# Performance work log

Measured on AMD Instinct MI355X. Metric: run time of the kernel, lower is better.

## Reference

```python
import jax, jax.numpy as jnp
import numpy as np

N = 100000      # nodes
E = 3200000     # edges
G = 128         # graphs in batch
D_IN = 128
D_H = 256
D_OUT = 64
BN_EPS = 1e-3


def setup_inputs() -> dict:
    key = jax.random.key(0)
    ks = jax.random.split(key, 12)
    h = jax.random.normal(ks[0], (N, D_IN), jnp.float32)
    src = jax.random.randint(ks[1], (E,), 0, N, jnp.int32)
    dst = jax.random.randint(ks[2], (E,), 0, N, jnp.int32)
    graph_ids = jnp.sort(jax.random.randint(ks[3], (N,), 0, G, jnp.int32))
    # GraphConv weights (DGL default: weight + bias)
    W0 = jax.random.normal(ks[4], (D_IN, D_H), jnp.float32) * 0.05
    b0 = jnp.zeros((D_H,), jnp.float32)
    W = jax.random.normal(ks[5], (2, D_H, D_H), jnp.float32) * 0.05  # layers 1,2
    b = jnp.zeros((2, D_H), jnp.float32)
    # BatchNorm1d params (eval mode: running stats), 3 norm layers
    bn_gamma = jnp.ones((3, D_H), jnp.float32)
    bn_beta = jnp.zeros((3, D_H), jnp.float32)
    bn_mean = jax.random.normal(ks[6], (3, D_H), jnp.float32) * 0.1
    bn_var = jax.random.uniform(ks[7], (3, D_H), jnp.float32, 0.5, 1.5)
    # prediction head
    Wp = jax.random.normal(ks[8], (D_H, D_OUT), jnp.float32) * 0.05
    bp = jnp.zeros((D_OUT,), jnp.float32)
    return {"h": h, "W0": W0, "b0": b0, "W": W, "b": b,
            "bn_gamma": bn_gamma, "bn_beta": bn_beta, "bn_mean": bn_mean,
            "bn_var": bn_var, "Wp": Wp, "bp": bp,
            "src": src, "dst": dst, "graph_ids": graph_ids}


def reference(h, W0, b0, W, b, bn_gamma, bn_beta, bn_mean, bn_var, Wp, bp,
              src, dst, graph_ids):
    n = h.shape[0]
    ones_e = jnp.ones(src.shape, h.dtype)
    # symmetric normalization (DGL GraphConv norm='both'), degrees clamped to 1
    out_deg = jax.ops.segment_sum(ones_e, src, num_segments=n)
    in_deg = jax.ops.segment_sum(ones_e, dst, num_segments=n)
    norm_src = jax.lax.rsqrt(jnp.clip(out_deg, 1.0))  # [N]
    norm_dst = jax.lax.rsqrt(jnp.clip(in_deg, 1.0))   # [N]

    def graph_conv(x, Wl, bl):
        x = (x * norm_src[:, None]) @ Wl              # transform first (mult W then aggregate)
        agg = jax.ops.segment_sum(x[src], dst, num_segments=n)  # SpMM: gather+scatter-add
        return agg * norm_dst[:, None] + bl

    Ws = [W0, W[0], W[1]]
    bs = [b0, b[0], b[1]]
    for i in range(3):
        x = h
        h = graph_conv(h, Ws[i], bs[i])
        # BatchNorm1d in eval mode (running stats), eps=1e-3
        h = (h - bn_mean[i]) * jax.lax.rsqrt(bn_var[i] + BN_EPS) * bn_gamma[i] + bn_beta[i]
        h = jax.nn.relu(h) + (x if i != 0 else 0.0)   # residual skipped on first layer

    # mean pooling per graph
    counts = jax.ops.segment_sum(jnp.ones((n,), h.dtype), graph_ids, num_segments=G)
    pooled = jax.ops.segment_sum(h, graph_ids, num_segments=G) / jnp.clip(counts, 1.0)[:, None]
    return pooled @ Wp + bp
```

## Files before the change

### kernel.cpp

```cpp
#include <hip/hip_runtime.h>
#include <hip/hip_bf16.h>

#define NN 100000
#define EE 3200000
#define GG 128
#define D_IN 128
#define D_H 256
#define D_OUT 64
#define BN_EPS 1e-3f
#define PAD 96
#define LDSTRIDE 40
#define X8SCALE 16.0f
#define X8INV   0.0625f

#define NBUCK 782
#define BUCKET_CAP 5120
#define EPT 8

#define GEMM_NWG 1564

typedef __hip_bfloat16 bf16;
typedef __attribute__((ext_vector_type(8))) short short8;
typedef __attribute__((ext_vector_type(4))) float float4v;
typedef __attribute__((ext_vector_type(2))) float float2v;
typedef __attribute__((ext_vector_type(4))) int intv4;
typedef __attribute__((ext_vector_type(4))) unsigned short usv4;

#if __has_builtin(__builtin_amdgcn_cvt_pk_f32_fp8) && __has_builtin(__builtin_amdgcn_cvt_pk_fp8_f32)
#define HAVE_FP8_CVT 1
#endif

__device__ inline float h2f(unsigned short s) {
    _Float16 h; __builtin_memcpy(&h, &s, 2); return (float)h;
}
__device__ inline unsigned short f2h(float f) {
    _Float16 h = (_Float16)f; unsigned short s; __builtin_memcpy(&s, &h, 2); return s;
}
__device__ inline float4 load4h(const unsigned short* p) {
    ushort4 u = *(const ushort4*)p;
    return make_float4(h2f(u.x), h2f(u.y), h2f(u.z), h2f(u.w));
}
__device__ inline void store4h(unsigned short* p, float4 v) {
    ushort4 u;
    u.x = f2h(v.x); u.y = f2h(v.y); u.z = f2h(v.z); u.w = f2h(v.w);
    *(ushort4*)p = u;
}
__device__ inline float4 load4h_nt(const unsigned short* p) {
    usv4 u = __builtin_nontemporal_load((const usv4*)p);
    return make_float4(h2f(u.x), h2f(u.y), h2f(u.z), h2f(u.w));
}

__device__ inline unsigned char enc_fp8(float f) {
#ifdef HAVE_FP8_CVT
    int r = __builtin_amdgcn_cvt_pk_fp8_f32(f, f, 0, false);
    return (unsigned char)(r & 0xFF);
#else
    union { float f; unsigned u; } c; c.f = f;
    unsigned s = (c.u >> 31) << 7;
    float a = fabsf(f);
    if (!(a >= 0.015625f)) {
        int q = (int)rintf(a * 512.0f);
        return (unsigned char)(s | (unsigned)q);
    }
    if (a >= 464.0f) return (unsigned char)(s | 0x7E);
    int e = (int)((c.u >> 23) & 0xFF) - 127;
    int q = (int)rintf(ldexpf(a, 3 - e));
    if (q == 16) { q = 8; e += 1; }
    return (unsigned char)(s | ((unsigned)(e + 7) << 3) | (unsigned)(q - 8));
#endif
}
__device__ inline unsigned int enc4_fp8(float4 v) {
#ifdef HAVE_FP8_CVT
    int r = __builtin_amdgcn_cvt_pk_fp8_f32(v.x, v.y, 0, false);
    r = __builtin_amdgcn_cvt_pk_fp8_f32(v.z, v.w, r, true);
    return (unsigned int)r;
#else
    return (unsigned int)enc_fp8(v.x) | ((unsigned int)enc_fp8(v.y) << 8)
         | ((unsigned int)enc_fp8(v.z) << 16) | ((unsigned int)enc_fp8(v.w) << 24);
#endif
}
__device__ inline float4 dec4_fp8(unsigned int w) {
#ifdef HAVE_FP8_CVT
    float2v lo = __builtin_amdgcn_cvt_pk_f32_fp8((int)w, false);
    float2v hi = __builtin_amdgcn_cvt_pk_f32_fp8((int)w, true);
    return make_float4(lo.x, lo.y, hi.x, hi.y);
#else
    float4 o;
    unsigned b0 = w & 0xFF, b1 = (w >> 8) & 0xFF, b2 = (w >> 16) & 0xFF, b3 = w >> 24;
    auto d1 = [](unsigned b) -> float {
        unsigned s = b >> 7, e = (b >> 3) & 0xF, m = b & 7;
        float v = e ? ldexpf((float)(8 + m), (int)e - 10) : ldexpf((float)m, -9);
        return s ? -v : v;
    };
    o.x = d1(b0); o.y = d1(b1); o.z = d1(b2); o.w = d1(b3);
    return o;
#endif
}

__device__ inline int xcd_swz_gemm(int bid) {
    int x = bid & 7, i = bid >> 3;
    return (x < 4 ? x * 196 : 784 + (x - 4) * 195) + i;
}

__global__ __launch_bounds__(1024) void k_bucket(const int* __restrict__ src,
                                                 const int* __restrict__ dst,
                                                 int* __restrict__ cursor,
                                                 int* __restrict__ scursor,
                                                 int* __restrict__ ebuf,
                                                 unsigned char* __restrict__ sbuf, int e) {
    __shared__ int hist[NBUCK];
    __shared__ int base[NBUCK];
    __shared__ int shist[NBUCK];
    __shared__ int sbase[NBUCK];
    int t = threadIdx.x;
    for (int i = t; i < NBUCK; i += 1024) { hist[i] = 0; shist[i] = 0; }
    __syncthreads();
    int e0 = blockIdx.x * (1024 * EPT) + t;
    int vals[EPT]; int bks[EPT]; int pk[EPT];
#pragma unroll
    for (int j = 0; j < EPT; ++j) {
        int idx = e0 + j * 1024;
        bks[j] = -1;
        if (idx < e) {
            int s = src[idx], d = dst[idx];
            bks[j] = d >> 7;
            vals[j] = (s << 7) | (d & 127);
            int r1 = atomicAdd(&hist[d >> 7], 1);
            int r2 = atomicAdd(&shist[s >> 7], 1);
            pk[j] = r1 | (r2 << 16);
        }
    }
    __syncthreads();
    for (int i = t; i < NBUCK; i += 1024) {
        int c = hist[i];
        base[i] = c ? atomicAdd(&cursor[i], c) : 0;
        int sc = shist[i];
        sbase[i] = sc ? atomicAdd(&scursor[i], sc) : 0;
    }
    __syncthreads();
#pragma unroll
    for (int j = 0; j < EPT; ++j) {
        if (bks[j] >= 0) {
            int v = vals[j];
            int rel = base[bks[j]] + (pk[j] & 0xFFFF);
            if (rel < BUCKET_CAP) ebuf[bks[j] * BUCKET_CAP + rel] = v;
            int sbk = v >> 14;
            int srel = sbase[sbk] + (pk[j] >> 16);
            if (srel < BUCKET_CAP) sbuf[(size_t)sbk * BUCKET_CAP + srel] = (unsigned char)((v >> 7) & 127);
        }
    }
}

__global__ __launch_bounds__(256) void k_fill(const int* __restrict__ cursor,
                                              const int* __restrict__ scursor,
                                              const int* __restrict__ ebuf,
                                              const unsigned char* __restrict__ sbuf,
                                              int* __restrict__ col_pad,
                                              int* __restrict__ deg_in,
                                              float* __restrict__ norm_src,
                                              float* __restrict__ norm_dst) {
    __shared__ int lcol[128 * PAD];
    __shared__ int ldeg[128];
    __shared__ int lodeg[128];
    int b = blockIdx.x;
    int t = threadIdx.x;
    if (t < 128) { ldeg[t] = 0; lodeg[t] = 0; }
    __syncthreads();
    int cnt = cursor[b]; if (cnt > BUCKET_CAP) cnt = BUCKET_CAP;
    const int* eb = ebuf + b * BUCKET_CAP;
    for (int i = t; i < cnt; i += 256) {
        int v = eb[i];
        int node = v & 127;
        int s = v >> 7;
        int pos = atomicAdd(&ldeg[node], 1);
        if (pos < PAD) lcol[node * PAD + pos] = s;
    }
    int scnt = scursor[b]; if (scnt > BUCKET_CAP) scnt = BUCKET_CAP;
    const unsigned char* sb = sbuf + (size_t)b * BUCKET_CAP;
    for (int i = t; i < scnt; i += 256) {
        atomicAdd(&lodeg[sb[i]], 1);
    }
    __syncthreads();
    int n0 = b << 7;
    int nn = NN - n0; if (nn > 128) nn = 128;
    int q = (nn * PAD) >> 2;
    int4* gdst = (int4*)(col_pad + (size_t)n0 * PAD);
    const int4* lsrc = (const int4*)lcol;
    for (int i = t; i < q; i += 256) gdst[i] = lsrc[i];
    if (t < nn) {
        int node = n0 + t;
        int din = ldeg[t];
        int dout = lodeg[t];
        deg_in[node] = din;
        norm_dst[node] = rsqrtf((float)(din < 1 ? 1 : din));
        norm_src[node] = rsqrtf((float)(dout < 1 ? 1 : dout));
    }
}

__global__ __launch_bounds__(256) void k_splitw(const float* __restrict__ W0,
                                                const float* __restrict__ Wl,
                                                unsigned short* __restrict__ wsplit) {
    int b = blockIdx.x;
    int n = threadIdx.x;
    const float* Wsrc; unsigned short* T; int K, k;
    if (b < 128)      { k = b;       K = 128; Wsrc = W0;          T = wsplit; }
    else if (b < 384) { k = b - 128; K = 256; Wsrc = Wl;          T = wsplit + 32768; }
    else              { k = b - 384; K = 256; Wsrc = Wl + 65536;  T = wsplit + 98304; }
    T[n * K + k] = f2h(Wsrc[k * 256 + n]);
}

__global__ __launch_bounds__(256) void k_convert(const float* __restrict__ h,
                                                 const float* __restrict__ norm_src,
                                                 unsigned int* __restrict__ xh8, int n) {
    int gid = blockIdx.x * 256 + threadIdx.x;
    int row = gid >> 5;
    int w = gid & 31;
    if (row < n) {
        float s = norm_src[row] * X8SCALE;
        float4 v = *(const float4*)(h + (size_t)row * D_IN + w * 4);
        v.x *= s; v.y *= s; v.z *= s; v.w *= s;
        xh8[(size_t)row * 32 + w] = enc4_fp8(v);
    }
}

__global__ __launch_bounds__(256) void k_spmm0(const unsigned char* __restrict__ x8,
                                               const int* __restrict__ deg_in,
                                               const int* __restrict__ col_pad,
                                               const float* __restrict__ norm_dst,
                                               unsigned short* __restrict__ p, int n) {
    int wv   = threadIdx.x >> 6;
    int lane = threadIdx.x & 63;
    int half = lane >> 5;
    int dl   = lane & 31;
    unsigned lb = (unsigned)dl << 2;
    int r = blockIdx.x * 8 + wv * 2 + half;
    if (r >= n) return;
    int d = deg_in[r]; if (d > PAD) d = PAD;
    int e0 = r * PAD, e1 = e0 + d;
    float ax = 0.f, ay = 0.f, az = 0.f, aw = 0.f;
    int e = e0;
    for (; e + 15 < e1; e += 16) {
        const intv4* cp = (const intv4*)(col_pad + e);
        intv4 i0 = __builtin_nontemporal_load(cp);
        intv4 i1 = __builtin_nontemporal_load(cp + 1);
        intv4 i2 = __builtin_nontemporal_load(cp + 2);
        intv4 i3 = __builtin_nontemporal_load(cp + 3);
        int s[16] = {i0.x, i0.y, i0.z, i0.w, i1.x, i1.y, i1.z, i1.w,
                     i2.x, i2.y, i2.z, i2.w, i3.x, i3.y, i3.z, i3.w};
        unsigned int w[16];
#pragma unroll
        for (int j = 0; j < 16; ++j)
            w[j] = *(const unsigned int*)(x8 + ((((unsigned)s[j]) << 7) | lb));
#pragma unroll
        for (int j = 0; j < 16; ++j) {
            float4 v = dec4_fp8(w[j]);
            ax += v.x; ay += v.y; az += v.z; aw += v.w;
        }
    }
    for (; e + 7 < e1; e += 8) {
        const intv4* cp = (const intv4*)(col_pad + e);
        intv4 i0 = __builtin_nontemporal_load(cp);
        intv4 i1 = __builtin_nontemporal_load(cp + 1);
        int s[8] = {i0.x, i0.y, i0.z, i0.w, i1.x, i1.y, i1.z, i1.w};
        unsigned int w[8];
#pragma unroll
        for (int j = 0; j < 8; ++j)
            w[j] = *(const unsigned int*)(x8 + ((((unsigned)s[j]) << 7) | lb));
#pragma unroll
        for (int j = 0; j < 8; ++j) {
            float4 v = dec4_fp8(w[j]);
            ax += v.x; ay += v.y; az += v.z; aw += v.w;
        }
    }
    for (; e < e1; ++e) {
        float4 v = dec4_fp8(*(const unsigned int*)(x8 + ((((unsigned)col_pad[e]) << 7) | lb)));
        ax += v.x; ay += v.y; az += v.z; aw += v.w;
    }
    float nd = norm_dst[r] * X8INV;
    store4h(p + (size_t)r * D_IN + dl * 4,
            make_float4(ax * nd, ay * nd, az * nd, aw * nd));
}

__global__ __launch_bounds__(256) void k_gemm_bn(const unsigned short* __restrict__ A,
                                                 const unsigned short* __restrict__ WT,
                                                 const float* __restrict__ bias,
                                                 const float* __restrict__ gamma,
                                                 const float* __restrict__ beta,
                                                 const float* __restrict__ mean,
                                                 const float* __restrict__ var,
                                                 unsigned short* __restrict__ H,
                                                 int M, int K) {
    __shared__ __align__(16) unsigned short lds[2 * 128 * LDSTRIDE];
    unsigned short* As = lds;
    unsigned short* Bf = lds + 128 * LDSTRIDE;
    int tid = threadIdx.x, wave = tid >> 6, lane = tid & 63, quad = lane >> 4, l15 = lane & 15;
    int sw = xcd_swz_gemm(blockIdx.x);
    int bm0 = (sw >> 1) * 128, bn0 = (sw & 1) * 128;
    int srow = tid >> 1, sseg = tid & 1;
    int agrow = bm0 + srow;
    float4v acc[2][8];
#pragma unroll
    for (int i = 0; i < 2; ++i)
#pragma unroll
        for (int j = 0; j < 8; ++j) acc[i][j] = (float4v){0.f, 0.f, 0.f, 0.f};

    for (int k0 = 0; k0 < K; k0 += 32) {
        ushort4 a0 = make_ushort4(0, 0, 0, 0), a1 = a0, a2 = a0, a3 = a0;
        if (agrow < M) {
            const ushort4* ap = (const ushort4*)(A + (size_t)agrow * K + k0 + sseg * 16);
            a0 = ap[0]; a1 = ap[1]; a2 = ap[2]; a3 = ap[3];
        }
        ushort4* ad = (ushort4*)&As[srow * LDSTRIDE + sseg * 16];
        ad[0] = a0; ad[1] = a1; ad[2] = a2; ad[3] = a3;
        const ushort4* wh = (const ushort4*)(WT + (size_t)(bn0 + srow) * K + k0 + sseg * 16);
        ushort4* bd = (ushort4*)&Bf[srow * LDSTRIDE + sseg * 16];
        bd[0] = wh[0]; bd[1] = wh[1]; bd[2] = wh[2]; bd[3] = wh[3];
        __syncthreads();
        short8 a0f = *(const short8*)&As[(wave * 32 + l15) * LDSTRIDE + quad * 8];
        short8 a1f = *(const short8*)&As[(wave * 32 + 16 + l15) * LDSTRIDE + quad * 8];
#pragma unroll
        for (int nt = 0; nt < 8; ++nt) {
            short8 bf = *(const short8*)&Bf[(nt * 16 + l15) * LDSTRIDE + quad * 8];
            acc[0][nt] = __builtin_amdgcn_mfma_f32_16x16x32_f16(a0f, bf, acc[0][nt], 0, 0, 0);
            acc[1][nt] = __builtin_amdgcn_mfma_f32_16x16x32_f16(a1f, bf, acc[1][nt], 0, 0, 0);
        }
        __syncthreads();
    }
#pragma unroll
    for (int nt = 0; nt < 8; ++nt) {
        int col = bn0 + nt * 16 + l15;
        float sc = rsqrtf(var[col] + BN_EPS) * gamma[col];
        float off = (bias[col] - mean[col]) * sc + beta[col];
#pragma unroll
        for (int rt = 0; rt < 2; ++rt) {
#pragma unroll
            for (int reg = 0; reg < 4; ++reg) {
                int m = bm0 + wave * 32 + rt * 16 + quad * 4 + reg;
                if (m < M) {
                    float o = fmaxf(acc[rt][nt][reg] * sc + off, 0.f);
                    H[(size_t)m * D_H + col] = f2h(o);
                }
            }
        }
    }
}

__global__ __launch_bounds__(256) void k_gemm_x(const unsigned short* __restrict__ A,
                                                const unsigned short* __restrict__ WT,
                                                const float* __restrict__ rowscale,
                                                unsigned char* __restrict__ X8,
                                                int M, int K) {
    __shared__ __align__(16) unsigned short lds[2 * 128 * LDSTRIDE];
    unsigned short* As = lds;
    unsigned short* Bf = lds + 128 * LDSTRIDE;
    int tid = threadIdx.x, wave = tid >> 6, lane = tid & 63, quad = lane >> 4, l15 = lane & 15;
    int sw = xcd_swz_gemm(blockIdx.x);
    int bm0 = (sw >> 1) * 128, bn0 = (sw & 1) * 128;
    int srow = tid >> 1, sseg = tid & 1;
    int agrow = bm0 + srow;
    float4v acc[2][8];
#pragma unroll
    for (int i = 0; i < 2; ++i)
#pragma unroll
        for (int j = 0; j < 8; ++j) acc[i][j] = (float4v){0.f, 0.f, 0.f, 0.f};

    for (int k0 = 0; k0 < K; k0 += 32) {
        ushort4 a0 = make_ushort4(0, 0, 0, 0), a1 = a0, a2 = a0, a3 = a0;
        if (agrow < M) {
            const ushort4* ap = (const ushort4*)(A + (size_t)agrow * K + k0 + sseg * 16);
            a0 = ap[0]; a1 = ap[1]; a2 = ap[2]; a3 = ap[3];
        }
        ushort4* ad = (ushort4*)&As[srow * LDSTRIDE + sseg * 16];
        ad[0] = a0; ad[1] = a1; ad[2] = a2; ad[3] = a3;
        const ushort4* wh = (const ushort4*)(WT + (size_t)(bn0 + srow) * K + k0 + sseg * 16);
        ushort4* bd = (ushort4*)&Bf[srow * LDSTRIDE + sseg * 16];
        bd[0] = wh[0]; bd[1] = wh[1]; bd[2] = wh[2]; bd[3] = wh[3];
        __syncthreads();
        short8 a0f = *(const short8*)&As[(wave * 32 + l15) * LDSTRIDE + quad * 8];
        short8 a1f = *(const short8*)&As[(wave * 32 + 16 + l15) * LDSTRIDE + quad * 8];
#pragma unroll
        for (int nt = 0; nt < 8; ++nt) {
            short8 bf = *(const short8*)&Bf[(nt * 16 + l15) * LDSTRIDE + quad * 8];
            acc[0][nt] = __builtin_amdgcn_mfma_f32_16x16x32_f16(a0f, bf, acc[0][nt], 0, 0, 0);
            acc[1][nt] = __builtin_amdgcn_mfma_f32_16x16x32_f16(a1f, bf, acc[1][nt], 0, 0, 0);
        }
        __syncthreads();
    }
#pragma unroll
    for (int rt = 0; rt < 2; ++rt) {
#pragma unroll
        for (int reg = 0; reg < 4; ++reg) {
            int m = bm0 + wave * 32 + rt * 16 + quad * 4 + reg;
            if (m < M) {
                float s = rowscale[m] * X8SCALE;
#pragma unroll
                for (int nt = 0; nt < 8; ++nt) {
                    int col = bn0 + nt * 16 + l15;
                    X8[(size_t)m * D_H + col] = enc_fp8(acc[rt][nt][reg] * s);
                }
            }
        }
    }
}

__global__ __launch_bounds__(256) void k_spmm12(const unsigned char* __restrict__ x8,
                                                const int* __restrict__ deg_in,
                                                const int* __restrict__ col_pad,
                                                const float* __restrict__ norm_dst,
                                                const float* __restrict__ bias,
                                                const float* __restrict__ gamma,
                                                const float* __restrict__ beta,
                                                const float* __restrict__ mean,
                                                const float* __restrict__ var,
                                                unsigned short* __restrict__ H, int n) {
    int wv = __builtin_amdgcn_readfirstlane(threadIdx.x >> 6);
    int r = blockIdx.x * 4 + wv;
    if (r >= n) return;
    int lane = threadIdx.x & 63;
    unsigned lb = (unsigned)lane << 2;
    int c = lane * 4;
    int d = deg_in[r]; if (d > PAD) d = PAD;
    int e0 = r * PAD, e1 = e0 + d;
    float ax = 0.f, ay = 0.f, az = 0.f, aw = 0.f;
    int e = e0;
    for (; e + 15 < e1; e += 16) {
        const intv4* cp = (const intv4*)(col_pad + e);
        intv4 i0 = __builtin_nontemporal_load(cp);
        intv4 i1 = __builtin_nontemporal_load(cp + 1);
        intv4 i2 = __builtin_nontemporal_load(cp + 2);
        intv4 i3 = __builtin_nontemporal_load(cp + 3);
        int s[16] = {i0.x, i0.y, i0.z, i0.w, i1.x, i1.y, i1.z, i1.w,
                     i2.x, i2.y, i2.z, i2.w, i3.x, i3.y, i3.z, i3.w};
        unsigned int w[16];
#pragma unroll
        for (int j = 0; j < 16; ++j)
            w[j] = *(const unsigned int*)(x8 + ((((unsigned)s[j]) << 8) | lb));
#pragma unroll
        for (int j = 0; j < 16; ++j) {
            float4 v = dec4_fp8(w[j]);
            ax += v.x; ay += v.y; az += v.z; aw += v.w;
        }
    }
    for (; e + 7 < e1; e += 8) {
        const intv4* cp = (const intv4*)(col_pad + e);
        intv4 i0 = __builtin_nontemporal_load(cp);
        intv4 i1 = __builtin_nontemporal_load(cp + 1);
        int s[8] = {i0.x, i0.y, i0.z, i0.w, i1.x, i1.y, i1.z, i1.w};
        unsigned int w[8];
#pragma unroll
        for (int j = 0; j < 8; ++j)
            w[j] = *(const unsigned int*)(x8 + ((((unsigned)s[j]) << 8) | lb));
#pragma unroll
        for (int j = 0; j < 8; ++j) {
            float4 v = dec4_fp8(w[j]);
            ax += v.x; ay += v.y; az += v.z; aw += v.w;
        }
    }
    for (; e < e1; ++e) {
        float4 v = dec4_fp8(*(const unsigned int*)(x8 + ((((unsigned)col_pad[e]) << 8) | lb)));
        ax += v.x; ay += v.y; az += v.z; aw += v.w;
    }
    float nd = norm_dst[r] * X8INV;
    float4 b4  = *(const float4*)(bias + c);
    float4 g4  = *(const float4*)(gamma + c);
    float4 be4 = *(const float4*)(beta + c);
    float4 m4  = *(const float4*)(mean + c);
    float4 v4  = *(const float4*)(var + c);
    float4 rv = load4h_nt(H + (size_t)r * D_H + c);
    float4 o;
    o.x = fmaxf((ax * nd + b4.x - m4.x) * rsqrtf(v4.x + BN_EPS) * g4.x + be4.x, 0.f) + rv.x;
    o.y = fmaxf((ay * nd + b4.y - m4.y) * rsqrtf(v4.y + BN_EPS) * g4.y + be4.y, 0.f) + rv.y;
    o.z = fmaxf((az * nd + b4.z - m4.z) * rsqrtf(v4.z + BN_EPS) * g4.z + be4.z, 0.f) + rv.z;
    o.w = fmaxf((aw * nd + b4.w - m4.w) * rsqrtf(v4.w + BN_EPS) * g4.w + be4.w, 0.f) + rv.w;
    store4h(H + (size_t)r * D_H + c, o);
}

__global__ __launch_bounds__(256) void k_pool(const unsigned short* __restrict__ h,
                                              const int* __restrict__ gid,
                                              float* __restrict__ pooled,
                                              float* __restrict__ counts, int n) {
    int wave = threadIdx.x >> 6;
    int lane = threadIdx.x & 63;
    int base = blockIdx.x * 256 + wave * 64;
    if (base >= n) return;
    int c = lane * 4;
    int end = base + 64; if (end > n) end = n;
    float ax = 0.f, ay = 0.f, az = 0.f, aw = 0.f;
    int cnt = 0, cur = -1;
    for (int i = base; i < end; ++i) {
        int g = gid[i];
        if (g != cur) {
            if (cnt > 0) {
                atomicAdd(&pooled[cur * D_H + c + 0], ax);
                atomicAdd(&pooled[cur * D_H + c + 1], ay);
                atomicAdd(&pooled[cur * D_H + c + 2], az);
                atomicAdd(&pooled[cur * D_H + c + 3], aw);
                if (lane == 0) atomicAdd(&counts[cur], (float)cnt);
            }
            cur = g; cnt = 0; ax = ay = az = aw = 0.f;
        }
        float4 v = load4h(h + (size_t)i * D_H + c);
        ax += v.x; ay += v.y; az += v.z; aw += v.w;
        cnt++;
    }
    if (cnt > 0) {
        atomicAdd(&pooled[cur * D_H + c + 0], ax);
        atomicAdd(&pooled[cur * D_H + c + 1], ay);
        atomicAdd(&pooled[cur * D_H + c + 2], az);
        atomicAdd(&pooled[cur * D_H + c + 3], aw);
        if (lane == 0) atomicAdd(&counts[cur], (float)cnt);
    }
}

__global__ __launch_bounds__(64) void k_head(const float* __restrict__ pooled,
                                             const float* __restrict__ counts,
                                             const float* __restrict__ Wp,
                                             const float* __restrict__ bp,
                                             float* __restrict__ out) {
    int g = blockIdx.x;
    int t = threadIdx.x;
    __shared__ float p[D_H];
    float inv = 1.0f / fmaxf(counts[g], 1.0f);
    for (int k = t; k < D_H; k += 64) p[k] = pooled[g * D_H + k] * inv;
    __syncthreads();
    float acc = bp[t];
#pragma unroll 8
    for (int k = 0; k < D_H; ++k) acc = fmaf(p[k], Wp[k * D_OUT + t], acc);
    out[g * D_OUT + t] = acc;
}

extern "C" void kernel_launch(void* const* d_in, const int* in_sizes, int n_in,
                              void* d_out, int out_size, void* d_ws, size_t ws_size,
                              hipStream_t stream) {
    (void)in_sizes; (void)n_in; (void)out_size; (void)ws_size;
    const float* h        = (const float*)d_in[0];
    const float* W0       = (const float*)d_in[1];
    const float* b0       = (const float*)d_in[2];
    const float* Wl       = (const float*)d_in[3];
    const float* bl       = (const float*)d_in[4];
    const float* bn_gamma = (const float*)d_in[5];
    const float* bn_beta  = (const float*)d_in[6];
    const float* bn_mean  = (const float*)d_in[7];
    const float* bn_var   = (const float*)d_in[8];
    const float* Wp       = (const float*)d_in[9];
    const float* bp       = (const float*)d_in[10];
    const int*   src      = (const int*)d_in[11];
    const int*   dst      = (const int*)d_in[12];
    const int*   gid      = (const int*)d_in[13];
    float* out = (float*)d_out;

    char* ws = (char*)d_ws;
    size_t off = 0;
    auto alloc = [&](size_t bytes) -> void* {
        void* p = ws + off;
        off += (bytes + 255) & ~(size_t)255;
        return p;
    };
    unsigned int*   bufXh8 = (unsigned int*)alloc((size_t)NN * D_IN);
    unsigned char*  bufX8  = (unsigned char*)alloc((size_t)NN * D_H);
    unsigned short* bufH   = (unsigned short*)alloc((size_t)NN * D_H * 2);
    unsigned short* bufP   = (unsigned short*)alloc((size_t)NN * D_IN * 2);
    int*   col_pad  = (int*)alloc(((size_t)NN * PAD + 64) * 4);
    float* norm_src = (float*)alloc((size_t)NN * 4);
    float* norm_dst = (float*)alloc((size_t)NN * 4);
    int*   degs     = (int*)alloc(((size_t)NN + 2 * NBUCK) * 4);
    int*   deg_in   = degs;
    int*   cursor   = degs + NN;
    int*   scursor  = degs + NN + NBUCK;
    unsigned short* wsplit = (unsigned short*)alloc(163840 * 2);
    float* pooled   = (float*)alloc((size_t)(GG * D_H + GG) * 4);
    float* counts   = pooled + GG * D_H;

    int* ebuf = (int*)bufX8;
    unsigned char* sbuf = (unsigned char*)bufH;

    unsigned short* w0T = wsplit;
    unsigned short* w1T = wsplit + 32768;
    unsigned short* w2T = wsplit + 98304;

    hipMemsetAsync(cursor, 0, (size_t)2 * NBUCK * 4, stream);
    hipMemsetAsync(pooled, 0, (size_t)(GG * D_H + GG) * 4, stream);

    const int NB = (NN + 255) / 256;
    const int SB = (NN + 3) / 4;
    const int SB0 = (NN + 7) / 8;

    k_splitw<<<640, 256, 0, stream>>>(W0, Wl, wsplit);
    k_bucket<<<(EE + 1024 * EPT - 1) / (1024 * EPT), 1024, 0, stream>>>(
        src, dst, cursor, scursor, ebuf, sbuf, EE);
    k_fill<<<NBUCK, 256, 0, stream>>>(cursor, scursor, ebuf, sbuf, col_pad, deg_in,
                                      norm_src, norm_dst);
    k_convert<<<(NN * 32 + 255) / 256, 256, 0, stream>>>(h, norm_src, bufXh8, NN);

    k_spmm0<<<SB0, 256, 0, stream>>>((const unsigned char*)bufXh8, deg_in, col_pad,
                                     norm_dst, bufP, NN);
    k_gemm_bn<<<GEMM_NWG, 256, 0, stream>>>(bufP, w0T, b0,
                                            bn_gamma, bn_beta, bn_mean, bn_var,
                                            bufH, NN, D_IN);
    k_gemm_x<<<GEMM_NWG, 256, 0, stream>>>(bufH, w1T, norm_src, bufX8, NN, D_H);
    k_spmm12<<<SB, 256, 0, stream>>>(bufX8, deg_in, col_pad, norm_dst, bl,
                                     bn_gamma + D_H, bn_beta + D_H,
                                     bn_mean + D_H, bn_var + D_H, bufH, NN);
    k_gemm_x<<<GEMM_NWG, 256, 0, stream>>>(bufH, w2T, norm_src, bufX8, NN, D_H);
    k_spmm12<<<SB, 256, 0, stream>>>(bufX8, deg_in, col_pad, norm_dst, bl + D_H,
                                     bn_gamma + 2 * D_H, bn_beta + 2 * D_H,
                                     bn_mean + 2 * D_H, bn_var + 2 * D_H, bufH, NN);

    k_pool<<<NB, 256, 0, stream>>>(bufH, gid, pooled, counts, NN);
    k_head<<<GG, 64, 0, stream>>>(pooled, counts, Wp, bp, out);
}
```

Measured before the change: 673.3 us.

## Fuse fp8 input conversion into fill and layer-0 SpMM into GEMM+BN

Folds the fp8 conversion of the input features into the CSR fill kernel, which already holds the out-degree counts, and drops the separate convert launch. Merges the layer-0 SpMM aggregation with the following GEMM+BatchNorm+ReLU kernel: each 512-thread block aggregates 128 rows into LDS and runs MFMA against the full 256-column weight. This removes the intermediate bf16 P buffer round-trip and two launches. In exchange, the aggregation and GEMM phases now serialize inside each block, and far fewer blocks (782 of 512 threads) run, which may reduce latency hiding for the gather.

```diff
diff --git a/kernel.cpp b/kernel.cpp
--- a/kernel.cpp
+++ b/kernel.cpp
@@ -10,6 +10,7 @@
 #define BN_EPS 1e-3f
 #define PAD 96
 #define LDSTRIDE 40
+#define AST 136
 #define X8SCALE 16.0f
 #define X8INV   0.0625f
 
@@ -151,14 +152,16 @@
     }
 }
 
-__global__ __launch_bounds__(256) void k_fill(const int* __restrict__ cursor,
+__global__ __launch_bounds__(512) void k_fill(const int* __restrict__ cursor,
                                               const int* __restrict__ scursor,
                                               const int* __restrict__ ebuf,
                                               const unsigned char* __restrict__ sbuf,
+                                              const float* __restrict__ h,
                                               int* __restrict__ col_pad,
                                               int* __restrict__ deg_in,
                                               float* __restrict__ norm_src,
-                                              float* __restrict__ norm_dst) {
+                                              float* __restrict__ norm_dst,
+                                              unsigned int* __restrict__ xh8) {
     __shared__ int lcol[128 * PAD];
     __shared__ int ldeg[128];
     __shared__ int lodeg[128];
@@ -168,7 +171,7 @@
     __syncthreads();
     int cnt = cursor[b]; if (cnt > BUCKET_CAP) cnt = BUCKET_CAP;
     const int* eb = ebuf + b * BUCKET_CAP;
-    for (int i = t; i < cnt; i += 256) {
+    for (int i = t; i < cnt; i += 512) {
         int v = eb[i];
         int node = v & 127;
         int s = v >> 7;
@@ -177,7 +180,7 @@
     }
     int scnt = scursor[b]; if (scnt > BUCKET_CAP) scnt = BUCKET_CAP;
     const unsigned char* sb = sbuf + (size_t)b * BUCKET_CAP;
-    for (int i = t; i < scnt; i += 256) {
+    for (int i = t; i < scnt; i += 512) {
         atomicAdd(&lodeg[sb[i]], 1);
     }
     __syncthreads();
@@ -186,7 +189,7 @@
     int q = (nn * PAD) >> 2;
     int4* gdst = (int4*)(col_pad + (size_t)n0 * PAD);
     const int4* lsrc = (const int4*)lcol;
-    for (int i = t; i < q; i += 256) gdst[i] = lsrc[i];
+    for (int i = t; i < q; i += 512) gdst[i] = lsrc[i];
     if (t < nn) {
         int node = n0 + t;
         int din = ldeg[t];
@@ -194,6 +197,14 @@
         deg_in[node] = din;
         norm_dst[node] = rsqrtf((float)(din < 1 ? 1 : din));
         norm_src[node] = rsqrtf((float)(dout < 1 ? 1 : dout));
+    }
+    for (int i = t; i < nn * 32; i += 512) {
+        int row = i >> 5, w = i & 31;
+        int dout = lodeg[row];
+        float s = rsqrtf((float)(dout < 1 ? 1 : dout)) * X8SCALE;
+        float4 v = *(const float4*)(h + (size_t)(n0 + row) * D_IN + w * 4);
+        v.x *= s; v.y *= s; v.z *= s; v.w *= s;
+        xh8[(size_t)(n0 + row) * 32 + w] = enc4_fp8(v);
     }
 }
 
@@ -209,137 +220,111 @@
     T[n * K + k] = f2h(Wsrc[k * 256 + n]);
 }
 
-__global__ __launch_bounds__(256) void k_convert(const float* __restrict__ h,
-                                                 const float* __restrict__ norm_src,
-                                                 unsigned int* __restrict__ xh8, int n) {
-    int gid = blockIdx.x * 256 + threadIdx.x;
-    int row = gid >> 5;
-    int w = gid & 31;
-    if (row < n) {
-        float s = norm_src[row] * X8SCALE;
-        float4 v = *(const float4*)(h + (size_t)row * D_IN + w * 4);
-        v.x *= s; v.y *= s; v.z *= s; v.w *= s;
-        xh8[(size_t)row * 32 + w] = enc4_fp8(v);
-    }
-}
-
-__global__ __launch_bounds__(256) void k_spmm0(const unsigned char* __restrict__ x8,
-                                               const int* __restrict__ deg_in,
-                                               const int* __restrict__ col_pad,
-                                               const float* __restrict__ norm_dst,
-                                               unsigned short* __restrict__ p, int n) {
-    int wv   = threadIdx.x >> 6;
-    int lane = threadIdx.x & 63;
-    int half = lane >> 5;
-    int dl   = lane & 31;
-    unsigned lb = (unsigned)dl << 2;
-    int r = blockIdx.x * 8 + wv * 2 + half;
-    if (r >= n) return;
-    int d = deg_in[r]; if (d > PAD) d = PAD;
-    int e0 = r * PAD, e1 = e0 + d;
-    float ax = 0.f, ay = 0.f, az = 0.f, aw = 0.f;
-    int e = e0;
-    for (; e + 15 < e1; e += 16) {
-        const intv4* cp = (const intv4*)(col_pad + e);
-        intv4 i0 = __builtin_nontemporal_load(cp);
-        intv4 i1 = __builtin_nontemporal_load(cp + 1);
-        intv4 i2 = __builtin_nontemporal_load(cp + 2);
-        intv4 i3 = __builtin_nontemporal_load(cp + 3);
-        int s[16] = {i0.x, i0.y, i0.z, i0.w, i1.x, i1.y, i1.z, i1.w,
-                     i2.x, i2.y, i2.z, i2.w, i3.x, i3.y, i3.z, i3.w};
-        unsigned int w[16];
-#pragma unroll
-        for (int j = 0; j < 16; ++j)
-            w[j] = *(const unsigned int*)(x8 + ((((unsigned)s[j]) << 7) | lb));
-#pragma unroll
-        for (int j = 0; j < 16; ++j) {
-            float4 v = dec4_fp8(w[j]);
-            ax += v.x; ay += v.y; az += v.z; aw += v.w;
-        }
-    }
-    for (; e + 7 < e1; e += 8) {
-        const intv4* cp = (const intv4*)(col_pad + e);
-        intv4 i0 = __builtin_nontemporal_load(cp);
-        intv4 i1 = __builtin_nontemporal_load(cp + 1);
-        int s[8] = {i0.x, i0.y, i0.z, i0.w, i1.x, i1.y, i1.z, i1.w};
-        unsigned int w[8];
-#pragma unroll
-        for (int j = 0; j < 8; ++j)
-            w[j] = *(const unsigned int*)(x8 + ((((unsigned)s[j]) << 7) | lb));
-#pragma unroll
-        for (int j = 0; j < 8; ++j) {
-            float4 v = dec4_fp8(w[j]);
-            ax += v.x; ay += v.y; az += v.z; aw += v.w;
-        }
-    }
-    for (; e < e1; ++e) {
-        float4 v = dec4_fp8(*(const unsigned int*)(x8 + ((((unsigned)col_pad[e]) << 7) | lb)));
-        ax += v.x; ay += v.y; az += v.z; aw += v.w;
-    }
-    float nd = norm_dst[r] * X8INV;
-    store4h(p + (size_t)r * D_IN + dl * 4,
-            make_float4(ax * nd, ay * nd, az * nd, aw * nd));
-}
-
-__global__ __launch_bounds__(256) void k_gemm_bn(const unsigned short* __restrict__ A,
+__global__ __launch_bounds__(512) void k_l0fused(const unsigned char* __restrict__ x8,
+                                                 const int* __restrict__ deg_in,
+                                                 const int* __restrict__ col_pad,
+                                                 const float* __restrict__ norm_dst,
                                                  const unsigned short* __restrict__ WT,
                                                  const float* __restrict__ bias,
                                                  const float* __restrict__ gamma,
                                                  const float* __restrict__ beta,
                                                  const float* __restrict__ mean,
                                                  const float* __restrict__ var,
-                                                 unsigned short* __restrict__ H,
-                                                 int M, int K) {
-    __shared__ __align__(16) unsigned short lds[2 * 128 * LDSTRIDE];
-    unsigned short* As = lds;
-    unsigned short* Bf = lds + 128 * LDSTRIDE;
-    int tid = threadIdx.x, wave = tid >> 6, lane = tid & 63, quad = lane >> 4, l15 = lane & 15;
-    int sw = xcd_swz_gemm(blockIdx.x);
-    int bm0 = (sw >> 1) * 128, bn0 = (sw & 1) * 128;
+                                                 unsigned short* __restrict__ H, int M) {
+    __shared__ __align__(16) unsigned short As[128 * AST];
+    __shared__ __align__(16) unsigned short Bf[256 * LDSTRIDE];
+    int tid = threadIdx.x;
+    int wv = tid >> 6;
+    int lane = tid & 63;
+    int half = lane >> 5;
+    int dl = lane & 31;
+    unsigned lb = (unsigned)dl << 2;
+    int bm0 = blockIdx.x * 128;
+
+    for (int p = 0; p < 8; ++p) {
+        int lr = p * 16 + wv * 2 + half;
+        int r = bm0 + lr;
+        if (r < M) {
+            int d = deg_in[r]; if (d > PAD) d = PAD;
+            int e0 = r * PAD, e1 = e0 + d;
+            float ax = 0.f, ay = 0.f, az = 0.f, aw = 0.f;
+            int e = e0;
+            for (; e + 15 < e1; e += 16) {
+                const intv4* cp = (const intv4*)(col_pad + e);
+                intv4 i0 = __builtin_nontemporal_load(cp);
+                intv4 i1 = __builtin_nontemporal_load(cp + 1);
+                intv4 i2 = __builtin_nontemporal_load(cp + 2);
+                intv4 i3 = __builtin_nontemporal_load(cp + 3);
+                int s[16] = {i0.x, i0.y, i0.z, i0.w, i1.x, i1.y, i1.z, i1.w,
+                             i2.x, i2.y, i2.z, i2.w, i3.x, i3.y, i3.z, i3.w};
+                unsigned int w[16];
+#pragma unroll
+                for (int j = 0; j < 16; ++j)
+                    w[j] = *(const unsigned int*)(x8 + ((((unsigned)s[j]) << 7) | lb));
+#pragma unroll
+                for (int j = 0; j < 16; ++j) {
+                    float4 v = dec4_fp8(w[j]);
+                    ax += v.x; ay += v.y; az += v.z; aw += v.w;
+                }
+            }
+            for (; e + 7 < e1; e += 8) {
+                const intv4* cp = (const intv4*)(col_pad + e);
+                intv4 i0 = __builtin_nontemporal_load(cp);
+                intv4 i1 = __builtin_nontemporal_load(cp + 1);
+                int s[8] = {i0.x, i0.y, i0.z, i0.w, i1.x, i1.y, i1.z, i1.w};
+                unsigned int w[8];
+#pragma unroll
+                for (int j = 0; j < 8; ++j)
+                    w[j] = *(const unsigned int*)(x8 + ((((unsigned)s[j]) << 7) | lb));
+#pragma unroll
+                for (int j = 0; j < 8; ++j) {
+                    float4 v = dec4_fp8(w[j]);
+                    ax += v.x; ay += v.y; az += v.z; aw += v.w;
+                }
+            }
+            for (; e < e1; ++e) {
+                float4 v = dec4_fp8(*(const unsigned int*)(x8 + ((((unsigned)col_pad[e]) << 7) | lb)));
+                ax += v.x; ay += v.y; az += v.z; aw += v.w;
+            }
+            float nd = norm_dst[r] * X8INV;
+            ushort4 u;
+            u.x = f2h(ax * nd); u.y = f2h(ay * nd); u.z = f2h(az * nd); u.w = f2h(aw * nd);
+            *(ushort4*)&As[lr * AST + dl * 4] = u;
+        }
+    }
+    __syncthreads();
+
+    int quad = lane >> 4, l15 = lane & 15;
     int srow = tid >> 1, sseg = tid & 1;
-    int agrow = bm0 + srow;
-    float4v acc[2][8];
-#pragma unroll
-    for (int i = 0; i < 2; ++i)
-#pragma unroll
-        for (int j = 0; j < 8; ++j) acc[i][j] = (float4v){0.f, 0.f, 0.f, 0.f};
-
-    for (int k0 = 0; k0 < K; k0 += 32) {
-        ushort4 a0 = make_ushort4(0, 0, 0, 0), a1 = a0, a2 = a0, a3 = a0;
-        if (agrow < M) {
-            const ushort4* ap = (const ushort4*)(A + (size_t)agrow * K + k0 + sseg * 16);
-            a0 = ap[0]; a1 = ap[1]; a2 = ap[2]; a3 = ap[3];
-        }
-        ushort4* ad = (ushort4*)&As[srow * LDSTRIDE + sseg * 16];
-        ad[0] = a0; ad[1] = a1; ad[2] = a2; ad[3] = a3;
-        const ushort4* wh = (const ushort4*)(WT + (size_t)(bn0 + srow) * K + k0 + sseg * 16);
+    float4v acc[16];
+#pragma unroll
+    for (int j = 0; j < 16; ++j) acc[j] = (float4v){0.f, 0.f, 0.f, 0.f};
+
+    for (int k0 = 0; k0 < 128; k0 += 32) {
+        const ushort4* wr = (const ushort4*)(WT + (size_t)srow * 128 + k0 + sseg * 16);
+        ushort4 b0 = wr[0], b1 = wr[1], b2 = wr[2], b3 = wr[3];
         ushort4* bd = (ushort4*)&Bf[srow * LDSTRIDE + sseg * 16];
-        bd[0] = wh[0]; bd[1] = wh[1]; bd[2] = wh[2]; bd[3] = wh[3];
+        bd[0] = b0; bd[1] = b1; bd[2] = b2; bd[3] = b3;
         __syncthreads();
-        short8 a0f = *(const short8*)&As[(wave * 32 + l15) * LDSTRIDE + quad * 8];
-        short8 a1f = *(const short8*)&As[(wave * 32 + 16 + l15) * LDSTRIDE + quad * 8];
-#pragma unroll
-        for (int nt = 0; nt < 8; ++nt) {
-            short8 bf = *(const short8*)&Bf[(nt * 16 + l15) * LDSTRIDE + quad * 8];
-            acc[0][nt] = __builtin_amdgcn_mfma_f32_16x16x32_f16(a0f, bf, acc[0][nt], 0, 0, 0);
-            acc[1][nt] = __builtin_amdgcn_mfma_f32_16x16x32_f16(a1f, bf, acc[1][nt], 0, 0, 0);
+        short8 a = *(const short8*)&As[(wv * 16 + l15) * AST + k0 + quad * 8];
+#pragma unroll
+        for (int nt = 0; nt < 16; ++nt) {
+            short8 bfr = *(const short8*)&Bf[(nt * 16 + l15) * LDSTRIDE + quad * 8];
+            acc[nt] = __builtin_amdgcn_mfma_f32_16x16x32_f16(a, bfr, acc[nt], 0, 0, 0);
         }
         __syncthreads();
     }
 #pragma unroll
-    for (int nt = 0; nt < 8; ++nt) {
-        int col = bn0 + nt * 16 + l15;
+    for (int nt = 0; nt < 16; ++nt) {
+        int col = nt * 16 + l15;
         float sc = rsqrtf(var[col] + BN_EPS) * gamma[col];
         float off = (bias[col] - mean[col]) * sc + beta[col];
 #pragma unroll
-        for (int rt = 0; rt < 2; ++rt) {
-#pragma unroll
-            for (int reg = 0; reg < 4; ++reg) {
-                int m = bm0 + wave * 32 + rt * 16 + quad * 4 + reg;
-                if (m < M) {
-                    float o = fmaxf(acc[rt][nt][reg] * sc + off, 0.f);
-                    H[(size_t)m * D_H + col] = f2h(o);
-                }
+        for (int reg = 0; reg < 4; ++reg) {
+            int m = bm0 + wv * 16 + quad * 4 + reg;
+            if (m < M) {
+                float o = fmaxf(acc[nt][reg] * sc + off, 0.f);
+                H[(size_t)m * D_H + col] = f2h(o);
             }
         }
     }
@@ -559,7 +544,6 @@
     unsigned int*   bufXh8 = (unsigned int*)alloc((size_t)NN * D_IN);
     unsigned char*  bufX8  = (unsigned char*)alloc((size_t)NN * D_H);
     unsigned short* bufH   = (unsigned short*)alloc((size_t)NN * D_H * 2);
-    unsigned short* bufP   = (unsigned short*)alloc((size_t)NN * D_IN * 2);
     int*   col_pad  = (int*)alloc(((size_t)NN * PAD + 64) * 4);
     float* norm_src = (float*)alloc((size_t)NN * 4);
     float* norm_dst = (float*)alloc((size_t)NN * 4);
@@ -583,20 +567,16 @@
 
     const int NB = (NN + 255) / 256;
     const int SB = (NN + 3) / 4;
-    const int SB0 = (NN + 7) / 8;
 
     k_splitw<<<640, 256, 0, stream>>>(W0, Wl, wsplit);
     k_bucket<<<(EE + 1024 * EPT - 1) / (1024 * EPT), 1024, 0, stream>>>(
         src, dst, cursor, scursor, ebuf, sbuf, EE);
-    k_fill<<<NBUCK, 256, 0, stream>>>(cursor, scursor, ebuf, sbuf, col_pad, deg_in,
-                                      norm_src, norm_dst);
-    k_convert<<<(NN * 32 + 255) / 256, 256, 0, stream>>>(h, norm_src, bufXh8, NN);
-
-    k_spmm0<<<SB0, 256, 0, stream>>>((const unsigned char*)bufXh8, deg_in, col_pad,
-                                     norm_dst, bufP, NN);
-    k_gemm_bn<<<GEMM_NWG, 256, 0, stream>>>(bufP, w0T, b0,
-                                            bn_gamma, bn_beta, bn_mean, bn_var,
-                                            bufH, NN, D_IN);
+    k_fill<<<NBUCK, 512, 0, stream>>>(cursor, scursor, ebuf, sbuf, h, col_pad, deg_in,
+                                      norm_src, norm_dst, bufXh8);
+
+    k_l0fused<<<NBUCK, 512, 0, stream>>>((const unsigned char*)bufXh8, deg_in, col_pad,
+                                         norm_dst, w0T, b0,
+                                         bn_gamma, bn_beta, bn_mean, bn_var, bufH, NN);
     k_gemm_x<<<GEMM_NWG, 256, 0, stream>>>(bufH, w1T, norm_src, bufX8, NN, D_H);
     k_spmm12<<<SB, 256, 0, stream>>>(bufX8, deg_in, col_pad, norm_dst, bl,
                                      bn_gamma + D_H, bn_beta + D_H,
```

New measurement: 705.2 us. +4.7%, slower.
